# Kernel tuning notes

Hardware: AMD Instinct MI355X
Metric: run time of the kernel (lower is better)

## Reference

```python
import jax, jax.numpy as jnp
import numpy as np

FEATURE_DIM = 1024
HEADS = 16
HEAD_DIM = FEATURE_DIM // HEADS


def setup_inputs() -> dict:
    key = jax.random.key(0)
    ks = jax.random.split(key, 9)
    B, C, T = 4, FEATURE_DIM, 4096
    s = 1.0 / np.sqrt(C)
    inp = {
        "x": jax.random.normal(ks[0], (B, C, T), dtype=jnp.float32),
        "Wq": jax.random.uniform(ks[1], (C, C), jnp.float32, -s, s),
        "bq": jax.random.uniform(ks[2], (C,), jnp.float32, -s, s),
        "Wk": jax.random.uniform(ks[3], (C, C), jnp.float32, -s, s),
        "bk": jax.random.uniform(ks[4], (C,), jnp.float32, -s, s),
        "Wv": jax.random.uniform(ks[5], (C, C), jnp.float32, -s, s),
        "bv": jax.random.uniform(ks[6], (C,), jnp.float32, -s, s),
        "Wo": jax.random.uniform(ks[7], (C, C), jnp.float32, -s, s),
        "bo": jax.random.uniform(ks[8], (C,), jnp.float32, -s, s),
    }
    return inp


def reference(x, Wq, bq, Wk, bk, Wv, bv, Wo, bo):
    B, C, T = x.shape
    H, D = HEADS, HEAD_DIM
    xt = jnp.transpose(x, (0, 2, 1))  # [B, T, C]
    # torch Linear: y = x @ W.T + b
    q = jax.nn.elu(xt @ Wq.T + bq).reshape(B, T, H, D) + 1.0
    k = jax.nn.elu(xt @ Wk.T + bk).reshape(B, T, H, D) + 1.0
    v = (xt @ Wv.T + bv).reshape(B, T, H, D)
    kv = jnp.einsum('bthd,bthe->bhde', k, v)      # [B, H, D, D]
    z = jnp.einsum('bthd,bhd->bth', q, k.sum(axis=1))  # [B, T, H]
    num = jnp.einsum('bthd,bhde->bthe', q, kv)    # [B, T, H, D]
    out = num / (z[..., None] + 1e-6)
    out = out.reshape(B, T, C)
    out = out @ Wo.T + bo  # dropout is identity in eval mode
    return jnp.transpose(out + xt, (0, 2, 1))  # [B, C, T]
```

## Files before the change

### kernel.cpp

```cpp
#include <hip/hip_runtime.h>
#include <hip/hip_bf16.h>
#include <cmath>

typedef unsigned short u16;
typedef unsigned int   u32;

#define BB 4
#define CC 1024
#define TT 4096
#define HH 16
#define DD 64

using bf16x8 = __attribute__((ext_vector_type(8))) __bf16;
using f32x4  = __attribute__((ext_vector_type(4))) float;

union FragU { bf16x8 v; u16 u[8]; };

__device__ __forceinline__ float bf2f(u16 u) {
    union { u32 i; float f; } v; v.i = ((u32)u) << 16; return v.f;
}
__device__ __forceinline__ u16 f2bf(float f) {
    union { float f; u32 i; } v; v.f = f;
    u32 x = v.i;
    return (u16)((x + 0x7fffu + ((x >> 16) & 1u)) >> 16);
}

__device__ __forceinline__ void gl_lds16(const u16* g, u16* l) {
    __builtin_amdgcn_global_load_lds(
        (const __attribute__((address_space(1))) void*)g,
        (__attribute__((address_space(3))) void*)l, 16, 0, 0);
}

__global__ __launch_bounds__(256) void cvt_kernel(
    const float* __restrict__ src, u16* __restrict__ dst, int n)
{
    const int i = (blockIdx.x * 256 + threadIdx.x) * 4;
    if (i < n) {
        const float4 v = *reinterpret_cast<const float4*>(src + i);
        ushort4 o;
        o.x = f2bf(v.x); o.y = f2bf(v.y); o.z = f2bf(v.z); o.w = f2bf(v.w);
        *reinterpret_cast<ushort4*>(dst + i) = o;
    }
}

__global__ __launch_bounds__(256) void transpose_kernel(
    const float* __restrict__ x, u16* __restrict__ xt)
{
    __shared__ u16 tile[64][65];
    const int b  = blockIdx.z;
    const int t0 = blockIdx.x * 64;
    const int c0 = blockIdx.y * 64;
    const float* xb  = x  + (size_t)b * CC * TT;
    u16*         xtb = xt + (size_t)b * TT * CC;
    #pragma unroll
    for (int p = 0; p < 16; ++p) {
        int idx = p * 256 + threadIdx.x;
        int r   = idx >> 6;
        int col = idx & 63;
        tile[r][col] = f2bf(xb[(size_t)(c0 + r) * TT + t0 + col]);
    }
    __syncthreads();
    #pragma unroll
    for (int p = 0; p < 16; ++p) {
        int idx = p * 256 + threadIdx.x;
        int r   = idx >> 6;
        int col = idx & 63;
        xtb[(size_t)(t0 + r) * CC + c0 + col] = tile[col][r];
    }
}

template <int MODE>
__global__ __launch_bounds__(256, 2) void gemm_kernel(
    const u16* __restrict__ A, const u16* __restrict__ W,
    const float* __restrict__ b0, const float* __restrict__ b1,
    const float* __restrict__ b2, u16* __restrict__ Ybf,
    float* __restrict__ Yf, const float* __restrict__ xres,
    int M, int N, int K)
{
    __shared__ u16 As[128 * 32];
    __shared__ u16 Ws[128 * 32];

    const int tid  = threadIdx.x;
    const int w    = tid >> 6;
    const int lane = tid & 63;
    const int wm = w >> 1, wn = w & 1;
    const int quad = lane >> 4, l16 = lane & 15;
    const int m0 = blockIdx.y * 128;
    const int n0 = blockIdx.x * 128;

    const int r0 = 32 * w + (lane >> 2);
    const int cB = (lane & 3) * 8;

    f32x4 acc[4][4];
    #pragma unroll
    for (int i = 0; i < 4; ++i)
        #pragma unroll
        for (int j = 0; j < 4; ++j) acc[i][j] = (f32x4)0.0f;

    for (int k0 = 0; k0 < K; k0 += 32) {
        __syncthreads();
        gl_lds16(A + (size_t)(m0 + r0) * K + k0 + cB,      &As[(32 * w) * 32]);
        gl_lds16(A + (size_t)(m0 + r0 + 16) * K + k0 + cB, &As[(32 * w + 16) * 32]);
        gl_lds16(W + (size_t)(n0 + r0) * K + k0 + cB,      &Ws[(32 * w) * 32]);
        gl_lds16(W + (size_t)(n0 + r0 + 16) * K + k0 + cB, &Ws[(32 * w + 16) * 32]);
        __syncthreads();

        bf16x8 af[4], bfr[4];
        #pragma unroll
        for (int i = 0; i < 4; ++i) {
            af[i]  = *reinterpret_cast<const bf16x8*>(&As[(wm * 64 + i * 16 + l16) * 32 + quad * 8]);
            bfr[i] = *reinterpret_cast<const bf16x8*>(&Ws[(wn * 64 + i * 16 + l16) * 32 + quad * 8]);
        }
        #pragma unroll
        for (int i = 0; i < 4; ++i)
            #pragma unroll
            for (int j = 0; j < 4; ++j)
                acc[i][j] = __builtin_amdgcn_mfma_f32_16x16x32_bf16(af[i], bfr[j], acc[i][j], 0, 0, 0);
    }

    if (MODE == 2) {
        const int b     = m0 / TT;
        const int tbase = m0 - b * TT;
        #pragma unroll
        for (int i = 0; i < 4; ++i) {
            const int t = tbase + wm * 64 + i * 16 + quad * 4;
            #pragma unroll
            for (int j = 0; j < 4; ++j) {
                const int col = n0 + wn * 64 + j * 16 + l16;
                const float bv = b0[col];
                const size_t base = ((size_t)b * CC + col) * TT + t;
                const float4 rx = *reinterpret_cast<const float4*>(&xres[base]);
                float4 o;
                o.x = acc[i][j][0] + bv + rx.x;
                o.y = acc[i][j][1] + bv + rx.y;
                o.z = acc[i][j][2] + bv + rx.z;
                o.w = acc[i][j][3] + bv + rx.w;
                *reinterpret_cast<float4*>(&Yf[base]) = o;
            }
        }
    } else {
        const int seg = n0 >> 10;
        const float* bp = (seg == 0) ? b0 : ((seg == 1) ? b1 : b2);
        u16* Yseg = Ybf + (size_t)seg * M * CC;
        #pragma unroll
        for (int i = 0; i < 4; ++i) {
            const int row = m0 + wm * 64 + i * 16 + quad * 4;
            #pragma unroll
            for (int j = 0; j < 4; ++j) {
                const int colL = (n0 & 1023) + wn * 64 + j * 16 + l16;
                const float bv = bp[colL];
                #pragma unroll
                for (int r = 0; r < 4; ++r) {
                    float v = acc[i][j][r] + bv;
                    if (seg < 2) v = (v > 0.0f) ? (v + 1.0f) : __expf(v);
                    Yseg[(size_t)(row + r) * CC + colL] = f2bf(v);
                }
            }
        }
    }
}

__global__ __launch_bounds__(256) void kv_kernel(
    const u16* __restrict__ Km, const u16* __restrict__ Vm,
    float* __restrict__ kv, float* __restrict__ ksum)
{
    __shared__ u16 Ks[32 * 64];
    __shared__ u16 Vs[32 * 64];
    const int bh = blockIdx.x;
    const int b = bh >> 4, h = bh & 15;
    const int tc0 = blockIdx.y * 512;
    const int tid = threadIdx.x;
    const int w = tid >> 6, lane = tid & 63;
    const int quad = lane >> 4, l16 = lane & 15;
    const u16* Kbase = Km + (size_t)b * TT * CC + h * DD;
    const u16* Vbase = Vm + (size_t)b * TT * CC + h * DD;

    const int srow = 8 * w + (lane >> 3);
    const int scol = (lane & 7) * 8;

    f32x4 acc[4];
    #pragma unroll
    for (int j = 0; j < 4; ++j) acc[j] = (f32x4)0.0f;
    f32x4 ks = (f32x4)0.0f;

    FragU ones;
    #pragma unroll
    for (int j = 0; j < 8; ++j) ones.u[j] = (l16 == 0) ? 0x3F80u : 0u;

    for (int c = 0; c < 16; ++c) {
        const int t0 = tc0 + 32 * c;
        __syncthreads();
        gl_lds16(Kbase + (size_t)(t0 + srow) * CC + scol, &Ks[8 * w * 64]);
        gl_lds16(Vbase + (size_t)(t0 + srow) * CC + scol, &Vs[8 * w * 64]);
        __syncthreads();

        FragU af;
        #pragma unroll
        for (int j = 0; j < 8; ++j)
            af.u[j] = Ks[(quad * 8 + j) * 64 + w * 16 + l16];
        #pragma unroll
        for (int e4 = 0; e4 < 4; ++e4) {
            FragU bf;
            #pragma unroll
            for (int j = 0; j < 8; ++j)
                bf.u[j] = Vs[(quad * 8 + j) * 64 + e4 * 16 + l16];
            acc[e4] = __builtin_amdgcn_mfma_f32_16x16x32_bf16(af.v, bf.v, acc[e4], 0, 0, 0);
        }
        ks = __builtin_amdgcn_mfma_f32_16x16x32_bf16(af.v, ones.v, ks, 0, 0, 0);
    }

    float* kvb = kv + (size_t)bh * DD * DD;
    #pragma unroll
    for (int e4 = 0; e4 < 4; ++e4)
        #pragma unroll
        for (int r = 0; r < 4; ++r)
            atomicAdd(&kvb[(w * 16 + quad * 4 + r) * DD + e4 * 16 + l16], acc[e4][r]);
    if (l16 == 0) {
        #pragma unroll
        for (int r = 0; r < 4; ++r)
            atomicAdd(&ksum[bh * DD + w * 16 + quad * 4 + r], ks[r]);
    }
}

__global__ __launch_bounds__(256) void attn_kernel(
    const u16* __restrict__ Q, const float* __restrict__ kv,
    const float* __restrict__ ksum, u16* __restrict__ attn)
{
    __shared__ float kvs[DD * DD];
    __shared__ float kss[DD];
    const int bh = blockIdx.x;
    const int b = bh >> 4, h = bh & 15;
    const int tb = blockIdx.y * 256;
    const int tid = threadIdx.x;
    const int w = tid >> 6, lane = tid & 63;
    const int quad = lane >> 4, l16 = lane & 15;

    const float* kvb = kv + (size_t)bh * DD * DD;
    {
        const float4* s4 = reinterpret_cast<const float4*>(kvb);
        float4* d4 = reinterpret_cast<float4*>(kvs);
        #pragma unroll
        for (int p = 0; p < 4; ++p) d4[p * 256 + tid] = s4[p * 256 + tid];
        if (tid < DD) kss[tid] = ksum[bh * DD + tid];
    }
    __syncthreads();

    FragU bf[4][2], zb[2];
    #pragma unroll
    for (int ck = 0; ck < 2; ++ck) {
        #pragma unroll
        for (int nt = 0; nt < 4; ++nt)
            #pragma unroll
            for (int j = 0; j < 8; ++j)
                bf[nt][ck].u[j] = f2bf(kvs[(ck * 32 + quad * 8 + j) * DD + nt * 16 + l16]);
        #pragma unroll
        for (int j = 0; j < 8; ++j)
            zb[ck].u[j] = (l16 == 0) ? f2bf(kss[ck * 32 + quad * 8 + j]) : 0u;
    }

    f32x4 acc[4][4], zacc[4];
    #pragma unroll
    for (int i = 0; i < 4; ++i) {
        zacc[i] = (f32x4)0.0f;
        #pragma unroll
        for (int j = 0; j < 4; ++j) acc[i][j] = (f32x4)0.0f;
    }

    const u16* Qbase = Q + ((size_t)b * TT) * CC + h * DD;
    #pragma unroll
    for (int i = 0; i < 4; ++i) {
        const int t = tb + w * 64 + i * 16 + l16;
        #pragma unroll
        for (int ck = 0; ck < 2; ++ck) {
            const bf16x8 af = *reinterpret_cast<const bf16x8*>(
                Qbase + (size_t)t * CC + ck * 32 + quad * 8);
            #pragma unroll
            for (int nt = 0; nt < 4; ++nt)
                acc[i][nt] = __builtin_amdgcn_mfma_f32_16x16x32_bf16(af, bf[nt][ck].v, acc[i][nt], 0, 0, 0);
            zacc[i] = __builtin_amdgcn_mfma_f32_16x16x32_bf16(af, zb[ck].v, zacc[i], 0, 0, 0);
        }
    }

    u16* obase = attn + ((size_t)b * TT) * CC + h * DD;
    #pragma unroll
    for (int i = 0; i < 4; ++i) {
        float inv[4];
        #pragma unroll
        for (int r = 0; r < 4; ++r) {
            const float zv = __shfl(zacc[i][r], lane & 48);
            inv[r] = 1.0f / (zv + 1e-6f);
        }
        #pragma unroll
        for (int nt = 0; nt < 4; ++nt) {
            #pragma unroll
            for (int r = 0; r < 4; ++r) {
                const int t = tb + w * 64 + i * 16 + quad * 4 + r;
                obase[(size_t)t * CC + nt * 16 + l16] = f2bf(acc[i][nt][r] * inv[r]);
            }
        }
    }
}

extern "C" void kernel_launch(void* const* d_in, const int* in_sizes, int n_in,
                              void* d_out, int out_size, void* d_ws, size_t ws_size,
                              hipStream_t stream)
{
    const float* x  = (const float*)d_in[0];
    const float* Wq = (const float*)d_in[1];
    const float* bq = (const float*)d_in[2];
    const float* Wk = (const float*)d_in[3];
    const float* bk = (const float*)d_in[4];
    const float* Wv = (const float*)d_in[5];
    const float* bv = (const float*)d_in[6];
    const float* Wo = (const float*)d_in[7];
    const float* bo = (const float*)d_in[8];
    float* out = (float*)d_out;

    const int M = BB * TT;
    const size_t BUF  = (size_t)BB * TT * CC * sizeof(u16);
    const size_t WBUF = (size_t)CC * CC * sizeof(u16);

    char* ws = (char*)d_ws;
    u16* xt   = (u16*)(ws);
    u16* Qb   = (u16*)(ws + BUF);
    u16* Wcat = (u16*)(ws + 4 * BUF);
    u16* Wob  = (u16*)(ws + 4 * BUF + 3 * WBUF);
    float* kvbuf = (float*)(ws + 4 * BUF + 4 * WBUF);
    float* ksumb = (float*)(ws + 4 * BUF + 4 * WBUF
                            + (size_t)BB * HH * DD * DD * sizeof(float));
    u16* attn = xt;

    hipMemsetAsync(kvbuf, 0,
        (size_t)(BB * HH * DD * DD + BB * HH * DD) * sizeof(float), stream);

    const int wn = CC * CC;
    cvt_kernel<<<wn / 1024, 256, 0, stream>>>(Wq, Wcat, wn);
    cvt_kernel<<<wn / 1024, 256, 0, stream>>>(Wk, Wcat + (size_t)wn, wn);
    cvt_kernel<<<wn / 1024, 256, 0, stream>>>(Wv, Wcat + 2 * (size_t)wn, wn);
    cvt_kernel<<<wn / 1024, 256, 0, stream>>>(Wo, Wob, wn);

    transpose_kernel<<<dim3(TT / 64, CC / 64, BB), 256, 0, stream>>>(x, xt);

    gemm_kernel<3><<<dim3(3 * CC / 128, M / 128), 256, 0, stream>>>(
        xt, Wcat, bq, bk, bv, Qb, nullptr, nullptr, M, 3 * CC, CC);

    kv_kernel<<<dim3(BB * HH, TT / 512), 256, 0, stream>>>(
        Qb + (size_t)M * CC, Qb + 2 * (size_t)M * CC, kvbuf, ksumb);

    attn_kernel<<<dim3(BB * HH, TT / 256), 256, 0, stream>>>(Qb, kvbuf, ksumb, attn);

    gemm_kernel<2><<<dim3(CC / 128, M / 128), 256, 0, stream>>>(
        attn, Wob, bo, nullptr, nullptr, nullptr, out, x, M, CC, CC);
}
```

Before: 373.3 us.

## Deepen GEMM K-tile with swizzled LDS, stage output GEMM epilogue, widen transpose

The GEMM now loads 64-wide K slices per iteration into XOR-swizzled shared memory, halving the number of barrier pairs and avoiding LDS bank conflicts on fragment reads. The output-projection epilogue stages accumulators through shared memory so each lane writes coalesced float4 runs along T for the residual add and store. The transpose kernel processes 256 channels per block and writes 32-bit packed pairs to cut store instructions. Shared memory per block grows to about 34 KB, which may limit occupancy.

```diff
diff --git a/kernel.cpp b/kernel.cpp
--- a/kernel.cpp
+++ b/kernel.cpp
@@ -46,26 +46,28 @@
 __global__ __launch_bounds__(256) void transpose_kernel(
     const float* __restrict__ x, u16* __restrict__ xt)
 {
-    __shared__ u16 tile[64][65];
+    __shared__ u16 tile[64 * 258];
     const int b  = blockIdx.z;
     const int t0 = blockIdx.x * 64;
-    const int c0 = blockIdx.y * 64;
+    const int c0 = blockIdx.y * 256;
     const float* xb  = x  + (size_t)b * CC * TT;
     u16*         xtb = xt + (size_t)b * TT * CC;
-    #pragma unroll
-    for (int p = 0; p < 16; ++p) {
-        int idx = p * 256 + threadIdx.x;
-        int r   = idx >> 6;
-        int col = idx & 63;
-        tile[r][col] = f2bf(xb[(size_t)(c0 + r) * TT + t0 + col]);
+
+    const int tcol = threadIdx.x & 63;
+    const int rw   = threadIdx.x >> 6;
+    #pragma unroll 8
+    for (int p = 0; p < 64; ++p) {
+        const int cr = p * 4 + rw;
+        tile[tcol * 258 + cr] = f2bf(xb[(size_t)(c0 + cr) * TT + t0 + tcol]);
     }
     __syncthreads();
-    #pragma unroll
-    for (int p = 0; p < 16; ++p) {
-        int idx = p * 256 + threadIdx.x;
-        int r   = idx >> 6;
-        int col = idx & 63;
-        xtb[(size_t)(t0 + r) * CC + c0 + col] = tile[col][r];
+    const int cp = threadIdx.x & 127;
+    const int th = threadIdx.x >> 7;
+    #pragma unroll 8
+    for (int q = 0; q < 32; ++q) {
+        const int tr = q * 2 + th;
+        const u32 v = *reinterpret_cast<const u32*>(&tile[tr * 258 + cp * 2]);
+        *reinterpret_cast<u32*>(&xtb[(size_t)(t0 + tr) * CC + c0 + cp * 2]) = v;
     }
 }
 
@@ -77,8 +79,9 @@
     float* __restrict__ Yf, const float* __restrict__ xres,
     int M, int N, int K)
 {
-    __shared__ u16 As[128 * 32];
-    __shared__ u16 Ws[128 * 32];
+    __shared__ char smem[34048];
+    u16* As = (u16*)smem;
+    u16* Ws = (u16*)(smem + 16384);
 
     const int tid  = threadIdx.x;
     const int w    = tid >> 6;
@@ -88,8 +91,8 @@
     const int m0 = blockIdx.y * 128;
     const int n0 = blockIdx.x * 128;
 
-    const int r0 = 32 * w + (lane >> 2);
-    const int cB = (lane & 3) * 8;
+    const int srow = lane >> 3;
+    const int scol = ((lane & 7) ^ srow) * 8;
 
     f32x4 acc[4][4];
     #pragma unroll
@@ -97,45 +100,68 @@
         #pragma unroll
         for (int j = 0; j < 4; ++j) acc[i][j] = (f32x4)0.0f;
 
-    for (int k0 = 0; k0 < K; k0 += 32) {
+    for (int k0 = 0; k0 < K; k0 += 64) {
         __syncthreads();
-        gl_lds16(A + (size_t)(m0 + r0) * K + k0 + cB,      &As[(32 * w) * 32]);
-        gl_lds16(A + (size_t)(m0 + r0 + 16) * K + k0 + cB, &As[(32 * w + 16) * 32]);
-        gl_lds16(W + (size_t)(n0 + r0) * K + k0 + cB,      &Ws[(32 * w) * 32]);
-        gl_lds16(W + (size_t)(n0 + r0 + 16) * K + k0 + cB, &Ws[(32 * w + 16) * 32]);
+        #pragma unroll
+        for (int s = 0; s < 4; ++s)
+            gl_lds16(A + (size_t)(m0 + 32 * w + 8 * s + srow) * K + k0 + scol,
+                     &As[(32 * w + 8 * s) * 64]);
+        #pragma unroll
+        for (int s = 0; s < 4; ++s)
+            gl_lds16(W + (size_t)(n0 + 32 * w + 8 * s + srow) * K + k0 + scol,
+                     &Ws[(32 * w + 8 * s) * 64]);
         __syncthreads();
 
-        bf16x8 af[4], bfr[4];
-        #pragma unroll
-        for (int i = 0; i < 4; ++i) {
-            af[i]  = *reinterpret_cast<const bf16x8*>(&As[(wm * 64 + i * 16 + l16) * 32 + quad * 8]);
-            bfr[i] = *reinterpret_cast<const bf16x8*>(&Ws[(wn * 64 + i * 16 + l16) * 32 + quad * 8]);
-        }
-        #pragma unroll
-        for (int i = 0; i < 4; ++i)
-            #pragma unroll
-            for (int j = 0; j < 4; ++j)
-                acc[i][j] = __builtin_amdgcn_mfma_f32_16x16x32_bf16(af[i], bfr[j], acc[i][j], 0, 0, 0);
+        #pragma unroll
+        for (int sub = 0; sub < 2; ++sub) {
+            const int pg = (((sub << 2) | quad) ^ (l16 & 7)) * 8;
+            bf16x8 af[4], bfr[4];
+            #pragma unroll
+            for (int i = 0; i < 4; ++i) {
+                af[i]  = *reinterpret_cast<const bf16x8*>(&As[(wm * 64 + i * 16 + l16) * 64 + pg]);
+                bfr[i] = *reinterpret_cast<const bf16x8*>(&Ws[(wn * 64 + i * 16 + l16) * 64 + pg]);
+            }
+            #pragma unroll
+            for (int i = 0; i < 4; ++i)
+                #pragma unroll
+                for (int j = 0; j < 4; ++j)
+                    acc[i][j] = __builtin_amdgcn_mfma_f32_16x16x32_bf16(af[i], bfr[j], acc[i][j], 0, 0, 0);
+        }
     }
 
     if (MODE == 2) {
+        float* Cs = (float*)smem;
         const int b     = m0 / TT;
         const int tbase = m0 - b * TT;
-        #pragma unroll
-        for (int i = 0; i < 4; ++i) {
-            const int t = tbase + wm * 64 + i * 16 + quad * 4;
-            #pragma unroll
-            for (int j = 0; j < 4; ++j) {
-                const int col = n0 + wn * 64 + j * 16 + l16;
-                const float bv = b0[col];
-                const size_t base = ((size_t)b * CC + col) * TT + t;
+        const int cl    = lane >> 4;
+        #pragma unroll
+        for (int hh = 0; hh < 2; ++hh) {
+            __syncthreads();
+            if (wm == hh) {
+                #pragma unroll
+                for (int i = 0; i < 4; ++i)
+                    #pragma unroll
+                    for (int j = 0; j < 4; ++j)
+                        #pragma unroll
+                        for (int r = 0; r < 4; ++r)
+                            Cs[(i * 16 + quad * 4 + r) * 133 + wn * 64 + j * 16 + l16] = acc[i][j][r];
+            }
+            __syncthreads();
+            #pragma unroll
+            for (int p = 0; p < 8; ++p) {
+                const int col = p * 16 + w * 4 + cl;
+                const int tl  = l16 * 4;
+                float4 v;
+                v.x = Cs[(tl + 0) * 133 + col];
+                v.y = Cs[(tl + 1) * 133 + col];
+                v.z = Cs[(tl + 2) * 133 + col];
+                v.w = Cs[(tl + 3) * 133 + col];
+                const float bv = b0[n0 + col];
+                const size_t base = ((size_t)b * CC + n0 + col) * TT + tbase + hh * 64 + tl;
                 const float4 rx = *reinterpret_cast<const float4*>(&xres[base]);
-                float4 o;
-                o.x = acc[i][j][0] + bv + rx.x;
-                o.y = acc[i][j][1] + bv + rx.y;
-                o.z = acc[i][j][2] + bv + rx.z;
-                o.w = acc[i][j][3] + bv + rx.w;
-                *reinterpret_cast<float4*>(&Yf[base]) = o;
+                v.x += bv + rx.x; v.y += bv + rx.y;
+                v.z += bv + rx.z; v.w += bv + rx.w;
+                *reinterpret_cast<float4*>(&Yf[base]) = v;
             }
         }
     } else {
@@ -339,7 +365,7 @@
     cvt_kernel<<<wn / 1024, 256, 0, stream>>>(Wv, Wcat + 2 * (size_t)wn, wn);
     cvt_kernel<<<wn / 1024, 256, 0, stream>>>(Wo, Wob, wn);
 
-    transpose_kernel<<<dim3(TT / 64, CC / 64, BB), 256, 0, stream>>>(x, xt);
+    transpose_kernel<<<dim3(TT / 64, CC / 256, BB), 256, 0, stream>>>(x, xt);
 
     gemm_kernel<3><<<dim3(3 * CC / 128, M / 128), 256, 0, stream>>>(
         xt, Wcat, bq, bk, bv, Qb, nullptr, nullptr, M, 3 * CC, CC);
```

New measurement: 358.0 us. 1.04x faster.
